# Optimization experiments

Hardware: AMD Instinct MI355X
Metric: run time of the kernel (lower is better)

## Reference

```python
import jax, jax.numpy as jnp
import numpy as np

N = 100000
E = 1600000
H = 2   # heads
C = 64  # per-head channels
NEG_SLOPE = 0.2


def setup_inputs() -> dict:
    key = jax.random.key(0)
    ks = jax.random.split(key, 12)
    s = 0.05
    return {
        "logits": jax.random.normal(ks[0], (N, 40), jnp.float32),
        "features": jax.random.normal(ks[1], (N, 256), jnp.float32),
        "edge_index": jax.random.randint(ks[2], (2, E), 0, N, jnp.int32),
        "W_feat": jax.random.normal(ks[3], (256, 128), jnp.float32) * s,
        "b_feat": jnp.zeros((128,), jnp.float32),
        "W0": jax.random.normal(ks[4], (168, 128), jnp.float32) * s,
        "att_src0": jax.random.normal(ks[5], (H, C), jnp.float32) * s,
        "att_dst0": jax.random.normal(ks[6], (H, C), jnp.float32) * s,
        "bias0": jnp.zeros((128,), jnp.float32),
        "W1": jax.random.normal(ks[7], (128, 128), jnp.float32) * s,
        "att_src1": jax.random.normal(ks[8], (H, C), jnp.float32) * s,
        "att_dst1": jax.random.normal(ks[9], (H, C), jnp.float32) * s,
        "bias1": jnp.zeros((128,), jnp.float32),
        "W_out": jax.random.normal(ks[10], (128, 40), jnp.float32) * s,
        "b_out": jnp.zeros((40,), jnp.float32),
    }


def gat_conv(x, src, dst, W, att_src, att_dst, bias):
    # x: [N, F_in] -> h: [N, H, C]
    h = (x @ W).reshape(N, H, C)
    a_src = (h * att_src).sum(-1)  # [N, H]
    a_dst = (h * att_dst).sum(-1)  # [N, H]
    # per-edge attention logits, leaky relu
    e = jax.nn.leaky_relu(a_src[src] + a_dst[dst], NEG_SLOPE)  # [E+N, H]
    # segment softmax over incoming edges of each dst node
    e_max = jax.ops.segment_max(e, dst, num_segments=N)
    e_exp = jnp.exp(e - e_max[dst])
    denom = jax.ops.segment_sum(e_exp, dst, num_segments=N)
    alpha = e_exp / (denom[dst] + 1e-16)  # [E+N, H]
    # weighted message aggregation (scatter-add)
    msg = h[src] * alpha[:, :, None]  # [E+N, H, C]
    out = jax.ops.segment_sum(msg, dst, num_segments=N)
    return out.reshape(N, H * C) + bias


def reference(logits, features, edge_index, W_feat, b_feat,
              W0, att_src0, att_dst0, bias0,
              W1, att_src1, att_dst1, bias1,
              W_out, b_out):
    # input assembly: [logits | proj(features)]
    x = jnp.concatenate([logits, features @ W_feat + b_feat], axis=-1)  # [N,168]
    # add self loops (PyG GATConv default add_self_loops=True)
    loops = jnp.arange(N, dtype=edge_index.dtype)
    src = jnp.concatenate([edge_index[0], loops])
    dst = jnp.concatenate([edge_index[1], loops])
    x = gat_conv(x, src, dst, W0, att_src0, att_dst0, bias0)
    x = jax.nn.relu(x)  # relu between conv layers (dropout=0 / eval)
    x = gat_conv(x, src, dst, W1, att_src1, att_dst1, bias1)
    return x @ W_out + b_out  # [N, 40]
```

## Files before the change

### kernel.cpp

```cpp
#include <hip/hip_runtime.h>

#define NN 100000
#define EE 1600000
#define NBUCK ((NN + 255) >> 8)
#define CHUNK 8192
#define NPBLK ((EE + CHUNK - 1) / CHUNK)

typedef __attribute__((ext_vector_type(8))) short short8_t;
typedef __attribute__((ext_vector_type(4))) float f32x4;

static __device__ inline unsigned short f2bf(float f) {
    unsigned int u = __float_as_uint(f);
    u += 0x7FFFu + ((u >> 16) & 1u);
    return (unsigned short)(u >> 16);
}
static __device__ inline float bf2f(unsigned short h) {
    return __uint_as_float(((unsigned int)h) << 16);
}

__global__ __launch_bounds__(256) void part_count(const int* __restrict__ ei,
                                                  int* __restrict__ cnt) {
    __shared__ int h[NBUCK];
    for (int i = threadIdx.x; i < NBUCK; i += 256) h[i] = 0;
    __syncthreads();
    int e0 = blockIdx.x * CHUNK;
    int e1 = e0 + CHUNK; if (e1 > EE) e1 = EE;
    for (int e = e0 + threadIdx.x; e < e1; e += 256)
        atomicAdd(&h[ei[EE + e] >> 8], 1);
    __syncthreads();
    for (int i = threadIdx.x; i < NBUCK; i += 256)
        cnt[blockIdx.x * NBUCK + i] = h[i];
}

__global__ void part_scan(const int* __restrict__ cnt, int* __restrict__ base,
                          int* __restrict__ bbase) {
    __shared__ int tot[512];
    int b = threadIdx.x;
    int t = 0;
    if (b < NBUCK)
        for (int k = 0; k < NPBLK; ++k) t += cnt[k * NBUCK + b];
    tot[b] = t;
    __syncthreads();
    for (int off = 1; off < 512; off <<= 1) {
        int u = (b >= off) ? tot[b - off] : 0;
        __syncthreads();
        tot[b] += u;
        __syncthreads();
    }
    int excl = tot[b] - t;
    if (b < NBUCK) {
        bbase[b] = excl;
        int run = excl;
        for (int k = 0; k < NPBLK; ++k) {
            base[k * NBUCK + b] = run;
            run += cnt[k * NBUCK + b];
        }
    }
    if (b == 0) bbase[NBUCK] = EE;
}

__global__ __launch_bounds__(256) void part_scatter(const int* __restrict__ ei,
                                                    const int* __restrict__ base,
                                                    unsigned int* __restrict__ bbuf) {
    __shared__ int lcur[NBUCK];
    for (int i = threadIdx.x; i < NBUCK; i += 256)
        lcur[i] = base[blockIdx.x * NBUCK + i];
    __syncthreads();
    int e0 = blockIdx.x * CHUNK;
    int e1 = e0 + CHUNK; if (e1 > EE) e1 = EE;
    for (int e = e0 + threadIdx.x; e < e1; e += 256) {
        int s = ei[e], d = ei[EE + e];
        int pos = atomicAdd(&lcur[d >> 8], 1);
        bbuf[pos] = (unsigned int)s | ((unsigned int)(d & 255) << 24);
    }
}

__global__ __launch_bounds__(256) void csr_build(const unsigned int* __restrict__ bbuf,
                                                 const int* __restrict__ bbase,
                                                 int* __restrict__ row_ptr,
                                                 int* __restrict__ col) {
    __shared__ int hist[256];
    __shared__ int sc[256];
    __shared__ int lcur[256];
    int b = blockIdx.x;
    int t = threadIdx.x;
    int n0 = b << 8;
    int nCnt = NN - n0; if (nCnt > 256) nCnt = 256;
    int es = bbase[b], ee2 = bbase[b + 1];
    hist[t] = 0;
    __syncthreads();
    for (int i = es + t; i < ee2; i += 256)
        atomicAdd(&hist[bbuf[i] >> 24], 1);
    __syncthreads();
    int v = hist[t];
    sc[t] = v;
    __syncthreads();
    for (int off = 1; off < 256; off <<= 1) {
        int u = (t >= off) ? sc[t - off] : 0;
        __syncthreads();
        sc[t] += u;
        __syncthreads();
    }
    int excl = sc[t] - v;
    if (t < nCnt) row_ptr[n0 + t] = es + excl;
    if (b == 0 && t == 0) row_ptr[NN] = EE;
    lcur[t] = excl;
    __syncthreads();
    for (int i = es + t; i < ee2; i += 256) {
        unsigned int pk = bbuf[i];
        int lpos = atomicAdd(&lcur[pk >> 24], 1);
        col[es + lpos] = (int)(pk & 0x00FFFFFFu);
    }
}

__global__ void bsplit_kernel(const float* __restrict__ W, int ldw, int K, int N,
                              unsigned short* __restrict__ BThi,
                              unsigned short* __restrict__ BTlo,
                              int stride, int koff, int KPseg) {
    int k = blockIdx.x * 256 + threadIdx.x;
    int col = blockIdx.y;
    if (k >= KPseg) return;
    float v = (k < K && col < N) ? W[(size_t)k * ldw + col] : 0.f;
    unsigned short hi = f2bf(v);
    unsigned short lo = f2bf(v - bf2f(hi));
    BThi[(size_t)col * stride + koff + k] = hi;
    BTlo[(size_t)col * stride + koff + k] = lo;
}

__global__ void cvec_kernel(const float* __restrict__ b_feat,
                            const float* __restrict__ W0, float* __restrict__ cvec) {
    int j = threadIdx.x;
    float s = 0.f;
    for (int k = 0; k < 128; ++k) s += b_feat[k] * W0[(40 + k) * 128 + j];
    cvec[j] = s;
}

#define AHI 0
#define ALO 2048
#define BHI 4096
#define BLO 8192
template <int OUTBF16, int ABF16>
__global__ __launch_bounds__(256) void mfma_gemm_kernel(
    const void* __restrict__ A1v, int lda1, int K1, int KP1,
    const float* __restrict__ A2, int lda2, int K2,
    int M,
    const unsigned short* __restrict__ BThi, const unsigned short* __restrict__ BTlo,
    int bstride, int KPtot,
    void* __restrict__ Cout, int ldc, int Nact, const float* __restrict__ bias)
{
    __shared__ __align__(16) unsigned short lds[12288];
    const int t = threadIdx.x;
    const int w = t >> 6, lane = t & 63;
    const int row0 = blockIdx.x * 64;
    const int rbase = (w & 1) * 32;
    const int cbase = (w >> 1) * 64;

    f32x4 acc[2][4];
#pragma unroll
    for (int i = 0; i < 2; ++i)
#pragma unroll
        for (int j = 0; j < 4; ++j) acc[i][j] = (f32x4){0.f, 0.f, 0.f, 0.f};

    const int arow = t >> 2;
    const int aslot = t & 3;
    const bool rowok = (row0 + arow) < M;
    const int aoff = arow * 32 + (((aslot ^ ((arow >> 1) & 3))) << 3);

    const int bc0 = t >> 2,        bs0 = t & 3;
    const int bc1 = (t + 256) >> 2, bs1 = (t + 256) & 3;
    const int bo0 = bc0 * 32 + ((bs0 ^ ((bc0 >> 1) & 3)) << 3);
    const int bo1 = bc1 * 32 + ((bs1 ^ ((bc1 >> 1) & 3)) << 3);

    float ra[8];
    short8_t rab;
    short8_t rbh0, rbl0, rbh1, rbl1;
    const short8_t zz = {0, 0, 0, 0, 0, 0, 0, 0};

#define LOADB(k0_) {                                                      \
        size_t g0_ = (size_t)bc0 * bstride + (k0_) + bs0 * 8;             \
        rbh0 = *(const short8_t*)&BThi[g0_];                              \
        rbl0 = *(const short8_t*)&BTlo[g0_];                              \
        size_t g1_ = (size_t)bc1 * bstride + (k0_) + bs1 * 8;             \
        rbh1 = *(const short8_t*)&BThi[g1_];                              \
        rbl1 = *(const short8_t*)&BTlo[g1_];                              \
    }

#define LOADA(k0_) {                                                      \
        if (ABF16) {                                                      \
            int gk = (k0_) + aslot * 8;                                   \
            if (rowok && gk + 8 <= K1) {                                  \
                const unsigned short* Ab =                                \
                    (const unsigned short*)A1v + (size_t)(row0 + arow) * lda1; \
                rab = *(const short8_t*)&Ab[gk];                          \
            } else rab = zz;                                              \
        } else {                                                          \
            const float* Asrc; int gk, Klim;                              \
            if ((k0_) < KP1) {                                            \
                Asrc = (const float*)A1v + (size_t)(row0 + arow) * lda1;  \
                gk = (k0_) + aslot * 8; Klim = K1;                        \
            } else {                                                      \
                Asrc = A2 + (size_t)(row0 + arow) * lda2;                 \
                gk = (k0_) - KP1 + aslot * 8; Klim = K2;                  \
            }                                                             \
            if (rowok && gk + 8 <= Klim) {                                \
                float4 v0 = *(const float4*)(Asrc + gk);                  \
                float4 v1 = *(const float4*)(Asrc + gk + 4);              \
                ra[0] = v0.x; ra[1] = v0.y; ra[2] = v0.z; ra[3] = v0.w;   \
                ra[4] = v1.x; ra[5] = v1.y; ra[6] = v1.z; ra[7] = v1.w;   \
            } else {                                                      \
                for (int j_ = 0; j_ < 8; ++j_) ra[j_] = 0.f;              \
            }                                                             \
        }                                                                 \
    }

    LOADA(0);
    LOADB(0);

    for (int k0 = 0; k0 < KPtot; k0 += 32) {
        if (ABF16) {
            *(short8_t*)&lds[AHI + aoff] = rab;
        } else {
            short8_t vh, vl;
#pragma unroll
            for (int j = 0; j < 8; ++j) {
                unsigned short hi = f2bf(ra[j]);
                vh[j] = (short)hi;
                vl[j] = (short)f2bf(ra[j] - bf2f(hi));
            }
            *(short8_t*)&lds[AHI + aoff] = vh;
            *(short8_t*)&lds[ALO + aoff] = vl;
        }
        *(short8_t*)&lds[BHI + bo0] = rbh0;
        *(short8_t*)&lds[BLO + bo0] = rbl0;
        *(short8_t*)&lds[BHI + bo1] = rbh1;
        *(short8_t*)&lds[BLO + bo1] = rbl1;
        __syncthreads();

        if (k0 + 32 < KPtot) {
            LOADA(k0 + 32);
            LOADB(k0 + 32);
        }

        short8_t Ah[2], Al[2], Bh[4], Bl[4];
        const int fslot = lane >> 4;
#pragma unroll
        for (int rt = 0; rt < 2; ++rt) {
            int r = rbase + rt * 16 + (lane & 15);
            int off = r * 32 + ((fslot ^ ((r >> 1) & 3)) << 3);
            Ah[rt] = *(const short8_t*)&lds[AHI + off];
            if (!ABF16) Al[rt] = *(const short8_t*)&lds[ALO + off];
        }
#pragma unroll
        for (int ct = 0; ct < 4; ++ct) {
            int c = cbase + ct * 16 + (lane & 15);
            int off = c * 32 + ((fslot ^ ((c >> 1) & 3)) << 3);
            Bh[ct] = *(const short8_t*)&lds[BHI + off];
            Bl[ct] = *(const short8_t*)&lds[BLO + off];
        }
#pragma unroll
        for (int rt = 0; rt < 2; ++rt)
#pragma unroll
            for (int ct = 0; ct < 4; ++ct) {
                acc[rt][ct] = __builtin_amdgcn_mfma_f32_16x16x32_bf16(Ah[rt], Bh[ct], acc[rt][ct], 0, 0, 0);
                acc[rt][ct] = __builtin_amdgcn_mfma_f32_16x16x32_bf16(Ah[rt], Bl[ct], acc[rt][ct], 0, 0, 0);
                if (!ABF16)
                    acc[rt][ct] = __builtin_amdgcn_mfma_f32_16x16x32_bf16(Al[rt], Bh[ct], acc[rt][ct], 0, 0, 0);
            }
        __syncthreads();
    }

#pragma unroll
    for (int rt = 0; rt < 2; ++rt) {
#pragma unroll
        for (int reg = 0; reg < 4; ++reg) {
            int r = row0 + rbase + rt * 16 + (lane >> 4) * 4 + reg;
            if (r >= M) continue;
#pragma unroll
            for (int ct = 0; ct < 4; ++ct) {
                int c = cbase + ct * 16 + (lane & 15);
                float v = acc[rt][ct][reg];
                if (bias) v += bias[c];
                if (OUTBF16) {
                    ((unsigned short*)Cout)[(size_t)r * 128 + c] = f2bf(v);
                } else {
                    if (c < Nact)
                        ((float*)Cout)[(size_t)r * ldc + c] = v;
                }
            }
        }
    }
#undef LOADA
#undef LOADB
}

__global__ void attn_coef_bf16(const unsigned short* __restrict__ hb,
                               const float* __restrict__ att_src,
                               const float* __restrict__ att_dst,
                               float* __restrict__ a_src, float* __restrict__ a_dst) {
    int n = (blockIdx.x * 256 + threadIdx.x) >> 6;
    if (n >= NN) return;
    int lane = threadIdx.x & 63;
    unsigned int hv = ((const unsigned int*)hb)[n * 64 + lane];
    float hx = __uint_as_float(hv << 16);
    float hy = __uint_as_float(hv & 0xFFFF0000u);
    int c0 = lane * 2;
    float vs = hx * att_src[c0] + hy * att_src[c0 + 1];
    float vd = hx * att_dst[c0] + hy * att_dst[c0 + 1];
#pragma unroll
    for (int off = 1; off <= 16; off <<= 1) {
        vs += __shfl_xor(vs, off);
        vd += __shfl_xor(vd, off);
    }
    if ((lane & 31) == 0) {
        int head = lane >> 5;
        a_src[n * 2 + head] = vs;
        a_dst[n * 2 + head] = vd;
    }
}

template <int RELU, int OUTBF16>
__global__ void gat_agg_fused(const int* __restrict__ row_ptr, const int* __restrict__ col,
                              const float* __restrict__ a_src, const float* __restrict__ a_dst,
                              const unsigned short* __restrict__ hb,
                              const float* __restrict__ bias, void* __restrict__ out) {
    int wid = (blockIdx.x * 256 + threadIdx.x) >> 6;
    if (wid >= NN) return;
    int lane = threadIdx.x & 63;
    int head = lane >> 5;
    const unsigned int* h2 = (const unsigned int*)hb;

    float2 ad = ((const float2*)a_dst)[wid];
    float2 asf = ((const float2*)a_src)[wid];
    float e0 = (head ? asf.y : asf.x) + (head ? ad.y : ad.x);
    e0 = e0 > 0.f ? e0 : 0.2f * e0;
    float w = __expf(e0);
    unsigned int hv = h2[wid * 64 + lane];
    float accx = w * __uint_as_float(hv << 16);
    float accy = w * __uint_as_float(hv & 0xFFFF0000u);
    float den = w;

    int rs = row_ptr[wid], re = row_ptr[wid + 1];
    for (int base = rs; base < re; base += 64) {
        int cnt = re - base;
        if (cnt > 64) cnt = 64;
        int sL = 0;
        float w0 = 0.f, w1 = 0.f;
        if (lane < cnt) {
            sL = col[base + lane];
            float2 as = ((const float2*)a_src)[sL];
            float t0 = as.x + ad.x;
            float t1 = as.y + ad.y;
            t0 = t0 > 0.f ? t0 : 0.2f * t0;
            t1 = t1 > 0.f ? t1 : 0.2f * t1;
            w0 = __expf(t0);
            w1 = __expf(t1);
        }
        int i = 0;
        for (; i + 8 <= cnt; i += 8) {
            int s[8];
            unsigned int g[8];
            float wa[8], wb[8];
#pragma unroll
            for (int j = 0; j < 8; ++j) s[j] = __shfl(sL, i + j);
#pragma unroll
            for (int j = 0; j < 8; ++j) g[j] = h2[s[j] * 64 + lane];
#pragma unroll
            for (int j = 0; j < 8; ++j) { wa[j] = __shfl(w0, i + j); wb[j] = __shfl(w1, i + j); }
#pragma unroll
            for (int j = 0; j < 8; ++j) {
                float ws = head ? wb[j] : wa[j];
                accx += ws * __uint_as_float(g[j] << 16);
                accy += ws * __uint_as_float(g[j] & 0xFFFF0000u);
                den += ws;
            }
        }
        for (; i + 4 <= cnt; i += 4) {
            int s[4];
            unsigned int g[4];
            float wa[4], wb[4];
#pragma unroll
            for (int j = 0; j < 4; ++j) s[j] = __shfl(sL, i + j);
#pragma unroll
            for (int j = 0; j < 4; ++j) g[j] = h2[s[j] * 64 + lane];
#pragma unroll
            for (int j = 0; j < 4; ++j) { wa[j] = __shfl(w0, i + j); wb[j] = __shfl(w1, i + j); }
#pragma unroll
            for (int j = 0; j < 4; ++j) {
                float ws = head ? wb[j] : wa[j];
                accx += ws * __uint_as_float(g[j] << 16);
                accy += ws * __uint_as_float(g[j] & 0xFFFF0000u);
                den += ws;
            }
        }
        for (; i < cnt; ++i) {
            int s = __shfl(sL, i);
            float wa = __shfl(w0, i);
            float wb = __shfl(w1, i);
            float ws = head ? wb : wa;
            unsigned int hs = h2[s * 64 + lane];
            accx += ws * __uint_as_float(hs << 16);
            accy += ws * __uint_as_float(hs & 0xFFFF0000u);
            den += ws;
        }
    }
    float inv = 1.f / (den + 1e-16f);
    float2 b2 = ((const float2*)bias)[lane];
    float ox = accx * inv + b2.x;
    float oy = accy * inv + b2.y;
    if (RELU) { ox = fmaxf(ox, 0.f); oy = fmaxf(oy, 0.f); }
    if (OUTBF16) {
        unsigned int pk = (unsigned int)f2bf(ox) | ((unsigned int)f2bf(oy) << 16);
        ((unsigned int*)out)[wid * 64 + lane] = pk;
    } else {
        ((float2*)out)[wid * 64 + lane] = make_float2(ox, oy);
    }
}

extern "C" void kernel_launch(void* const* d_in, const int* in_sizes, int n_in,
                              void* d_out, int out_size, void* d_ws, size_t ws_size,
                              hipStream_t stream) {
    const float* logits   = (const float*)d_in[0];
    const float* features = (const float*)d_in[1];
    const int*   ei       = (const int*)d_in[2];
    const float* W_feat   = (const float*)d_in[3];
    const float* b_feat   = (const float*)d_in[4];
    const float* W0       = (const float*)d_in[5];
    const float* att_src0 = (const float*)d_in[6];
    const float* att_dst0 = (const float*)d_in[7];
    const float* bias0    = (const float*)d_in[8];
    const float* W1       = (const float*)d_in[9];
    const float* att_src1 = (const float*)d_in[10];
    const float* att_dst1 = (const float*)d_in[11];
    const float* bias1    = (const float*)d_in[12];
    const float* W_out    = (const float*)d_in[13];
    const float* b_out    = (const float*)d_in[14];
    float* out = (float*)d_out;

    float* agg    = (float*)d_ws;
    float* a_srcb = agg + (size_t)NN * 128;
    float* a_dstb = a_srcb + (size_t)NN * 2;
    float* Wc     = a_dstb + (size_t)NN * 2;
    float* cvec   = Wc + 256 * 128;
    unsigned short* hbuf = (unsigned short*)(cvec + 128);
    unsigned short* BT0hi = hbuf + (size_t)NN * 128;
    unsigned short* BT0lo = BT0hi + 128 * 320;
    unsigned short* BTbhi = BT0lo + 128 * 320;
    unsigned short* BTblo = BTbhi + 128 * 128;
    unsigned short* BT1hi = BTblo + 128 * 128;
    unsigned short* BT1lo = BT1hi + 128 * 128;
    unsigned short* BTohi = BT1lo + 128 * 128;
    unsigned short* BTolo = BTohi + 128 * 128;
    int* row_ptr = (int*)(BTolo + 128 * 128);
    int* colbuf  = row_ptr + NN + 1;
    int* cnt     = colbuf + EE;
    int* pbase   = cnt + NPBLK * NBUCK;
    int* bbase   = pbase + NPBLK * NBUCK;
    unsigned int* bbuf = (unsigned int*)agg;
    unsigned short* aggb = (unsigned short*)agg;

    dim3 blk(256);
    const int gemmGrid = (NN + 63) / 64;
    const int nodeWaveGrid = (NN + 3) / 4;

    part_count<<<dim3(NPBLK), blk, 0, stream>>>(ei, cnt);
    part_scan<<<dim3(1), dim3(512), 0, stream>>>(cnt, pbase, bbase);
    part_scatter<<<dim3(NPBLK), blk, 0, stream>>>(ei, pbase, bbuf);
    csr_build<<<dim3(NBUCK), blk, 0, stream>>>(bbuf, bbase, row_ptr, colbuf);

    bsplit_kernel<<<dim3(1, 128), blk, 0, stream>>>(W0, 128, 40, 128, BT0hi, BT0lo, 320, 0, 64);
    bsplit_kernel<<<dim3(1, 128), blk, 0, stream>>>(W0 + 40 * 128, 128, 128, 128, BTbhi, BTblo, 128, 0, 128);
    mfma_gemm_kernel<0, 0><<<dim3(4), blk, 0, stream>>>(
        W_feat, 128, 128, 128, nullptr, 0, 0, 256,
        BTbhi, BTblo, 128, 128, Wc, 128, 128, nullptr);
    cvec_kernel<<<dim3(1), dim3(128), 0, stream>>>(b_feat, W0, cvec);
    bsplit_kernel<<<dim3(1, 128), blk, 0, stream>>>(Wc, 128, 256, 128, BT0hi, BT0lo, 320, 64, 256);
    bsplit_kernel<<<dim3(1, 128), blk, 0, stream>>>(W1, 128, 128, 128, BT1hi, BT1lo, 128, 0, 128);
    bsplit_kernel<<<dim3(1, 128), blk, 0, stream>>>(W_out, 40, 128, 40, BTohi, BTolo, 128, 0, 128);

    mfma_gemm_kernel<1, 0><<<dim3(gemmGrid), blk, 0, stream>>>(
        logits, 40, 40, 64, features, 256, 256, NN,
        BT0hi, BT0lo, 320, 320, hbuf, 128, 128, cvec);
    attn_coef_bf16<<<dim3(nodeWaveGrid), blk, 0, stream>>>(hbuf, att_src0, att_dst0, a_srcb, a_dstb);
    gat_agg_fused<1, 1><<<dim3(nodeWaveGrid), blk, 0, stream>>>(
        row_ptr, colbuf, a_srcb, a_dstb, hbuf, bias0, aggb);

    mfma_gemm_kernel<1, 1><<<dim3(gemmGrid), blk, 0, stream>>>(
        aggb, 128, 128, 128, nullptr, 0, 0, NN,
        BT1hi, BT1lo, 128, 128, hbuf, 128, 128, nullptr);
    attn_coef_bf16<<<dim3(nodeWaveGrid), blk, 0, stream>>>(hbuf, att_src1, att_dst1, a_srcb, a_dstb);
    gat_agg_fused<0, 0><<<dim3(nodeWaveGrid), blk, 0, stream>>>(
        row_ptr, colbuf, a_srcb, a_dstb, hbuf, bias1, agg);

    mfma_gemm_kernel<0, 0><<<dim3(gemmGrid), blk, 0, stream>>>(
        agg, 128, 128, 128, nullptr, 0, 0, NN,
        BTohi, BTolo, 128, 128, out, 40, 40, b_out);
}
```

Before: 332.5 us.

## Fuse attention coefficients into GEMM epilogue, double-buffer k-loop, trim output GEMM tiles

Attention-coefficient dot products are now computed in the MFMA GEMM epilogue from fp32 accumulators, which removes two separate kernels that re-read the bf16 h buffer. The GEMM k-loop is unrolled by two with two register prefetch buffers. The 40-column output GEMM uses a narrower column tile (NCT=2) so it skips unused B columns. The aggregation kernel now has each half-wave compute only its own head's edge weights over 32-edge chunks, which halves the exp work but doubles the number of chunk iterations. Attention coefficients now come from unrounded fp32 values instead of bf16 h, which slightly changes numerics, and the extra prefetch buffers raise register pressure.

```diff
diff --git a/kernel.cpp b/kernel.cpp
--- a/kernel.cpp
+++ b/kernel.cpp
@@ -139,60 +139,65 @@
 #define ALO 2048
 #define BHI 4096
 #define BLO 8192
-template <int OUTBF16, int ABF16>
+template <int OUTBF16, int ABF16, int ATTN, int NCT>
 __global__ __launch_bounds__(256) void mfma_gemm_kernel(
     const void* __restrict__ A1v, int lda1, int K1, int KP1,
     const float* __restrict__ A2, int lda2, int K2,
     int M,
     const unsigned short* __restrict__ BThi, const unsigned short* __restrict__ BTlo,
     int bstride, int KPtot,
-    void* __restrict__ Cout, int ldc, int Nact, const float* __restrict__ bias)
+    void* __restrict__ Cout, int ldc, int Nact, const float* __restrict__ bias,
+    const float* __restrict__ att_src, const float* __restrict__ att_dst,
+    float* __restrict__ a_srcO, float* __restrict__ a_dstO)
 {
     __shared__ __align__(16) unsigned short lds[12288];
     const int t = threadIdx.x;
     const int w = t >> 6, lane = t & 63;
     const int row0 = blockIdx.x * 64;
     const int rbase = (w & 1) * 32;
-    const int cbase = (w >> 1) * 64;
-
-    f32x4 acc[2][4];
+    const int cbase = (NCT == 4) ? (w >> 1) * 64 : (w >> 1) * 32;
+
+    f32x4 acc[2][NCT];
 #pragma unroll
     for (int i = 0; i < 2; ++i)
 #pragma unroll
-        for (int j = 0; j < 4; ++j) acc[i][j] = (f32x4){0.f, 0.f, 0.f, 0.f};
+        for (int j = 0; j < NCT; ++j) acc[i][j] = (f32x4){0.f, 0.f, 0.f, 0.f};
 
     const int arow = t >> 2;
     const int aslot = t & 3;
     const bool rowok = (row0 + arow) < M;
     const int aoff = arow * 32 + (((aslot ^ ((arow >> 1) & 3))) << 3);
 
-    const int bc0 = t >> 2,        bs0 = t & 3;
+    const int bc0 = t >> 2,         bs0 = t & 3;
     const int bc1 = (t + 256) >> 2, bs1 = (t + 256) & 3;
     const int bo0 = bc0 * 32 + ((bs0 ^ ((bc0 >> 1) & 3)) << 3);
     const int bo1 = bc1 * 32 + ((bs1 ^ ((bc1 >> 1) & 3)) << 3);
 
-    float ra[8];
-    short8_t rab;
-    short8_t rbh0, rbl0, rbh1, rbl1;
+    float ra0[8], ra1[8];
+    short8_t rab0, rab1;
+    short8_t bh0a, bl0a, bh1a, bl1a;
+    short8_t bh0b, bl0b, bh1b, bl1b;
     const short8_t zz = {0, 0, 0, 0, 0, 0, 0, 0};
 
-#define LOADB(k0_) {                                                      \
+#define LOADB_(k0_, H0, L0, H1, L1) {                                     \
         size_t g0_ = (size_t)bc0 * bstride + (k0_) + bs0 * 8;             \
-        rbh0 = *(const short8_t*)&BThi[g0_];                              \
-        rbl0 = *(const short8_t*)&BTlo[g0_];                              \
-        size_t g1_ = (size_t)bc1 * bstride + (k0_) + bs1 * 8;             \
-        rbh1 = *(const short8_t*)&BThi[g1_];                              \
-        rbl1 = *(const short8_t*)&BTlo[g1_];                              \
-    }
-
-#define LOADA(k0_) {                                                      \
+        H0 = *(const short8_t*)&BThi[g0_];                                \
+        L0 = *(const short8_t*)&BTlo[g0_];                                \
+        if (NCT == 4) {                                                   \
+            size_t g1_ = (size_t)bc1 * bstride + (k0_) + bs1 * 8;         \
+            H1 = *(const short8_t*)&BThi[g1_];                            \
+            L1 = *(const short8_t*)&BTlo[g1_];                            \
+        }                                                                 \
+    }
+
+#define LOADA_(k0_, RA, RAB) {                                            \
         if (ABF16) {                                                      \
             int gk = (k0_) + aslot * 8;                                   \
             if (rowok && gk + 8 <= K1) {                                  \
                 const unsigned short* Ab =                                \
                     (const unsigned short*)A1v + (size_t)(row0 + arow) * lda1; \
-                rab = *(const short8_t*)&Ab[gk];                          \
-            } else rab = zz;                                              \
+                RAB = *(const short8_t*)&Ab[gk];                          \
+            } else RAB = zz;                                              \
         } else {                                                          \
             const float* Asrc; int gk, Klim;                              \
             if ((k0_) < KP1) {                                            \
@@ -205,67 +210,81 @@
             if (rowok && gk + 8 <= Klim) {                                \
                 float4 v0 = *(const float4*)(Asrc + gk);                  \
                 float4 v1 = *(const float4*)(Asrc + gk + 4);              \
-                ra[0] = v0.x; ra[1] = v0.y; ra[2] = v0.z; ra[3] = v0.w;   \
-                ra[4] = v1.x; ra[5] = v1.y; ra[6] = v1.z; ra[7] = v1.w;   \
+                RA[0] = v0.x; RA[1] = v0.y; RA[2] = v0.z; RA[3] = v0.w;   \
+                RA[4] = v1.x; RA[5] = v1.y; RA[6] = v1.z; RA[7] = v1.w;   \
             } else {                                                      \
-                for (int j_ = 0; j_ < 8; ++j_) ra[j_] = 0.f;              \
+                for (int j_ = 0; j_ < 8; ++j_) RA[j_] = 0.f;              \
             }                                                             \
         }                                                                 \
     }
 
-    LOADA(0);
-    LOADB(0);
-
-    for (int k0 = 0; k0 < KPtot; k0 += 32) {
-        if (ABF16) {
-            *(short8_t*)&lds[AHI + aoff] = rab;
-        } else {
-            short8_t vh, vl;
-#pragma unroll
-            for (int j = 0; j < 8; ++j) {
-                unsigned short hi = f2bf(ra[j]);
-                vh[j] = (short)hi;
-                vl[j] = (short)f2bf(ra[j] - bf2f(hi));
-            }
-            *(short8_t*)&lds[AHI + aoff] = vh;
-            *(short8_t*)&lds[ALO + aoff] = vl;
-        }
-        *(short8_t*)&lds[BHI + bo0] = rbh0;
-        *(short8_t*)&lds[BLO + bo0] = rbl0;
-        *(short8_t*)&lds[BHI + bo1] = rbh1;
-        *(short8_t*)&lds[BLO + bo1] = rbl1;
-        __syncthreads();
-
-        if (k0 + 32 < KPtot) {
-            LOADA(k0 + 32);
-            LOADB(k0 + 32);
-        }
-
-        short8_t Ah[2], Al[2], Bh[4], Bl[4];
-        const int fslot = lane >> 4;
-#pragma unroll
-        for (int rt = 0; rt < 2; ++rt) {
-            int r = rbase + rt * 16 + (lane & 15);
-            int off = r * 32 + ((fslot ^ ((r >> 1) & 3)) << 3);
-            Ah[rt] = *(const short8_t*)&lds[AHI + off];
-            if (!ABF16) Al[rt] = *(const short8_t*)&lds[ALO + off];
-        }
-#pragma unroll
-        for (int ct = 0; ct < 4; ++ct) {
-            int c = cbase + ct * 16 + (lane & 15);
-            int off = c * 32 + ((fslot ^ ((c >> 1) & 3)) << 3);
-            Bh[ct] = *(const short8_t*)&lds[BHI + off];
-            Bl[ct] = *(const short8_t*)&lds[BLO + off];
-        }
-#pragma unroll
-        for (int rt = 0; rt < 2; ++rt)
-#pragma unroll
-            for (int ct = 0; ct < 4; ++ct) {
-                acc[rt][ct] = __builtin_amdgcn_mfma_f32_16x16x32_bf16(Ah[rt], Bh[ct], acc[rt][ct], 0, 0, 0);
-                acc[rt][ct] = __builtin_amdgcn_mfma_f32_16x16x32_bf16(Ah[rt], Bl[ct], acc[rt][ct], 0, 0, 0);
-                if (!ABF16)
-                    acc[rt][ct] = __builtin_amdgcn_mfma_f32_16x16x32_bf16(Al[rt], Bh[ct], acc[rt][ct], 0, 0, 0);
-            }
+#define STAGE_(RA, RAB, H0, L0, H1, L1) {                                 \
+        if (ABF16) {                                                      \
+            *(short8_t*)&lds[AHI + aoff] = RAB;                           \
+        } else {                                                          \
+            short8_t vh_, vl_;                                            \
+            for (int j_ = 0; j_ < 8; ++j_) {                              \
+                unsigned short hi_ = f2bf(RA[j_]);                        \
+                vh_[j_] = (short)hi_;                                     \
+                vl_[j_] = (short)f2bf(RA[j_] - bf2f(hi_));                \
+            }                                                             \
+            *(short8_t*)&lds[AHI + aoff] = vh_;                           \
+            *(short8_t*)&lds[ALO + aoff] = vl_;                           \
+        }                                                                 \
+        *(short8_t*)&lds[BHI + bo0] = H0;                                 \
+        *(short8_t*)&lds[BLO + bo0] = L0;                                 \
+        if (NCT == 4) {                                                   \
+            *(short8_t*)&lds[BHI + bo1] = H1;                             \
+            *(short8_t*)&lds[BLO + bo1] = L1;                             \
+        }                                                                 \
+    }
+
+#define COMPUTE_() {                                                      \
+        short8_t Ah[2], Al[2], Bh[NCT], Bl[NCT];                          \
+        const int fslot = lane >> 4;                                      \
+        for (int rt = 0; rt < 2; ++rt) {                                  \
+            int r = rbase + rt * 16 + (lane & 15);                        \
+            int off = r * 32 + ((fslot ^ ((r >> 1) & 3)) << 3);           \
+            Ah[rt] = *(const short8_t*)&lds[AHI + off];                   \
+            if (!ABF16) Al[rt] = *(const short8_t*)&lds[ALO + off];       \
+        }                                                                 \
+        for (int ct = 0; ct < NCT; ++ct) {                                \
+            int c = cbase + ct * 16 + (lane & 15);                        \
+            int off = c * 32 + ((fslot ^ ((c >> 1) & 3)) << 3);           \
+            Bh[ct] = *(const short8_t*)&lds[BHI + off];                   \
+            Bl[ct] = *(const short8_t*)&lds[BLO + off];                   \
+        }                                                                 \
+        for (int rt = 0; rt < 2; ++rt)                                    \
+            for (int ct = 0; ct < NCT; ++ct) {                            \
+                acc[rt][ct] = __builtin_amdgcn_mfma_f32_16x16x32_bf16(Ah[rt], Bh[ct], acc[rt][ct], 0, 0, 0); \
+                acc[rt][ct] = __builtin_amdgcn_mfma_f32_16x16x32_bf16(Ah[rt], Bl[ct], acc[rt][ct], 0, 0, 0); \
+                if (!ABF16)                                               \
+                    acc[rt][ct] = __builtin_amdgcn_mfma_f32_16x16x32_bf16(Al[rt], Bh[ct], acc[rt][ct], 0, 0, 0); \
+            }                                                             \
+    }
+
+    LOADA_(0, ra0, rab0);
+    LOADB_(0, bh0a, bl0a, bh1a, bl1a);
+    LOADA_(32, ra1, rab1);
+    LOADB_(32, bh0b, bl0b, bh1b, bl1b);
+
+    for (int k0 = 0; k0 < KPtot; k0 += 64) {
+        STAGE_(ra0, rab0, bh0a, bl0a, bh1a, bl1a);
+        __syncthreads();
+        if (k0 + 64 < KPtot) {
+            LOADA_(k0 + 64, ra0, rab0);
+            LOADB_(k0 + 64, bh0a, bl0a, bh1a, bl1a);
+        }
+        COMPUTE_();
+        __syncthreads();
+
+        STAGE_(ra1, rab1, bh0b, bl0b, bh1b, bl1b);
+        __syncthreads();
+        if (k0 + 96 < KPtot) {
+            LOADA_(k0 + 96, ra1, rab1);
+            LOADB_(k0 + 96, bh0b, bl0b, bh1b, bl1b);
+        }
+        COMPUTE_();
         __syncthreads();
     }
 
@@ -274,9 +293,28 @@
 #pragma unroll
         for (int reg = 0; reg < 4; ++reg) {
             int r = row0 + rbase + rt * 16 + (lane >> 4) * 4 + reg;
+            if (ATTN) {
+                float ps = 0.f, pd = 0.f;
+#pragma unroll
+                for (int ct = 0; ct < NCT; ++ct) {
+                    int c = cbase + ct * 16 + (lane & 15);
+                    ps += acc[rt][ct][reg] * att_src[c];
+                    pd += acc[rt][ct][reg] * att_dst[c];
+                }
+#pragma unroll
+                for (int off = 1; off < 16; off <<= 1) {
+                    ps += __shfl_xor(ps, off);
+                    pd += __shfl_xor(pd, off);
+                }
+                if (r < M && (lane & 15) == 0) {
+                    int head = w >> 1;
+                    a_srcO[r * 2 + head] = ps;
+                    a_dstO[r * 2 + head] = pd;
+                }
+            }
             if (r >= M) continue;
 #pragma unroll
-            for (int ct = 0; ct < 4; ++ct) {
+            for (int ct = 0; ct < NCT; ++ct) {
                 int c = cbase + ct * 16 + (lane & 15);
                 float v = acc[rt][ct][reg];
                 if (bias) v += bias[c];
@@ -289,33 +327,10 @@
             }
         }
     }
-#undef LOADA
-#undef LOADB
-}
-
-__global__ void attn_coef_bf16(const unsigned short* __restrict__ hb,
-                               const float* __restrict__ att_src,
-                               const float* __restrict__ att_dst,
-                               float* __restrict__ a_src, float* __restrict__ a_dst) {
-    int n = (blockIdx.x * 256 + threadIdx.x) >> 6;
-    if (n >= NN) return;
-    int lane = threadIdx.x & 63;
-    unsigned int hv = ((const unsigned int*)hb)[n * 64 + lane];
-    float hx = __uint_as_float(hv << 16);
-    float hy = __uint_as_float(hv & 0xFFFF0000u);
-    int c0 = lane * 2;
-    float vs = hx * att_src[c0] + hy * att_src[c0 + 1];
-    float vd = hx * att_dst[c0] + hy * att_dst[c0 + 1];
-#pragma unroll
-    for (int off = 1; off <= 16; off <<= 1) {
-        vs += __shfl_xor(vs, off);
-        vd += __shfl_xor(vd, off);
-    }
-    if ((lane & 31) == 0) {
-        int head = lane >> 5;
-        a_src[n * 2 + head] = vs;
-        a_dst[n * 2 + head] = vd;
-    }
+#undef LOADA_
+#undef LOADB_
+#undef STAGE_
+#undef COMPUTE_
 }
 
 template <int RELU, int OUTBF16>
@@ -326,77 +341,73 @@
     int wid = (blockIdx.x * 256 + threadIdx.x) >> 6;
     if (wid >= NN) return;
     int lane = threadIdx.x & 63;
-    int head = lane >> 5;
+    int hc = lane >> 5;
     const unsigned int* h2 = (const unsigned int*)hb;
 
     float2 ad = ((const float2*)a_dst)[wid];
     float2 asf = ((const float2*)a_src)[wid];
-    float e0 = (head ? asf.y : asf.x) + (head ? ad.y : ad.x);
+    float adh = hc ? ad.y : ad.x;
+    float e0 = (hc ? asf.y : asf.x) + adh;
     e0 = e0 > 0.f ? e0 : 0.2f * e0;
     float w = __expf(e0);
     unsigned int hv = h2[wid * 64 + lane];
     float accx = w * __uint_as_float(hv << 16);
     float accy = w * __uint_as_float(hv & 0xFFFF0000u);
     float den = w;
+    const int shbase = hc << 5;
 
     int rs = row_ptr[wid], re = row_ptr[wid + 1];
-    for (int base = rs; base < re; base += 64) {
+    for (int base = rs; base < re; base += 32) {
         int cnt = re - base;
-        if (cnt > 64) cnt = 64;
+        if (cnt > 32) cnt = 32;
+        int eidx = lane & 31;
         int sL = 0;
-        float w0 = 0.f, w1 = 0.f;
-        if (lane < cnt) {
-            sL = col[base + lane];
+        float wL = 0.f;
+        if (eidx < cnt) {
+            sL = col[base + eidx];
             float2 as = ((const float2*)a_src)[sL];
-            float t0 = as.x + ad.x;
-            float t1 = as.y + ad.y;
-            t0 = t0 > 0.f ? t0 : 0.2f * t0;
-            t1 = t1 > 0.f ? t1 : 0.2f * t1;
-            w0 = __expf(t0);
-            w1 = __expf(t1);
+            float tt = (hc ? as.y : as.x) + adh;
+            tt = tt > 0.f ? tt : 0.2f * tt;
+            wL = __expf(tt);
         }
         int i = 0;
         for (; i + 8 <= cnt; i += 8) {
             int s[8];
             unsigned int g[8];
-            float wa[8], wb[8];
-#pragma unroll
-            for (int j = 0; j < 8; ++j) s[j] = __shfl(sL, i + j);
+            float ws[8];
+#pragma unroll
+            for (int j = 0; j < 8; ++j) s[j] = __shfl(sL, shbase + i + j);
 #pragma unroll
             for (int j = 0; j < 8; ++j) g[j] = h2[s[j] * 64 + lane];
 #pragma unroll
-            for (int j = 0; j < 8; ++j) { wa[j] = __shfl(w0, i + j); wb[j] = __shfl(w1, i + j); }
+            for (int j = 0; j < 8; ++j) ws[j] = __shfl(wL, shbase + i + j);
 #pragma unroll
             for (int j = 0; j < 8; ++j) {
-                float ws = head ? wb[j] : wa[j];
-                accx += ws * __uint_as_float(g[j] << 16);
-                accy += ws * __uint_as_float(g[j] & 0xFFFF0000u);
-                den += ws;
+                accx += ws[j] * __uint_as_float(g[j] << 16);
+                accy += ws[j] * __uint_as_float(g[j] & 0xFFFF0000u);
+                den += ws[j];
             }
         }
         for (; i + 4 <= cnt; i += 4) {
             int s[4];
             unsigned int g[4];
-            float wa[4], wb[4];
-#pragma unroll
-            for (int j = 0; j < 4; ++j) s[j] = __shfl(sL, i + j);
+            float ws[4];
+#pragma unroll
+            for (int j = 0; j < 4; ++j) s[j] = __shfl(sL, shbase + i + j);
 #pragma unroll
             for (int j = 0; j < 4; ++j) g[j] = h2[s[j] * 64 + lane];
 #pragma unroll
-            for (int j = 0; j < 4; ++j) { wa[j] = __shfl(w0, i + j); wb[j] = __shfl(w1, i + j); }
+            for (int j = 0; j < 4; ++j) ws[j] = __shfl(wL, shbase + i + j);
 #pragma unroll
             for (int j = 0; j < 4; ++j) {
-                float ws = head ? wb[j] : wa[j];
-                accx += ws * __uint_as_float(g[j] << 16);
-                accy += ws * __uint_as_float(g[j] & 0xFFFF0000u);
-                den += ws;
+                accx += ws[j] * __uint_as_float(g[j] << 16);
+                accy += ws[j] * __uint_as_float(g[j] & 0xFFFF0000u);
+                den += ws[j];
             }
         }
         for (; i < cnt; ++i) {
-            int s = __shfl(sL, i);
-            float wa = __shfl(w0, i);
-            float wb = __shfl(w1, i);
-            float ws = head ? wb : wa;
+            int s = __shfl(sL, shbase + i);
+            float ws = __shfl(wL, shbase + i);
             unsigned int hs = h2[s * 64 + lane];
             accx += ws * __uint_as_float(hs << 16);
             accy += ws * __uint_as_float(hs & 0xFFFF0000u);
@@ -469,29 +480,31 @@
 
     bsplit_kernel<<<dim3(1, 128), blk, 0, stream>>>(W0, 128, 40, 128, BT0hi, BT0lo, 320, 0, 64);
     bsplit_kernel<<<dim3(1, 128), blk, 0, stream>>>(W0 + 40 * 128, 128, 128, 128, BTbhi, BTblo, 128, 0, 128);
-    mfma_gemm_kernel<0, 0><<<dim3(4), blk, 0, stream>>>(
+    mfma_gemm_kernel<0, 0, 0, 4><<<dim3(4), blk, 0, stream>>>(
         W_feat, 128, 128, 128, nullptr, 0, 0, 256,
-        BTbhi, BTblo, 128, 128, Wc, 128, 128, nullptr);
+        BTbhi, BTblo, 128, 128, Wc, 128, 128, nullptr,
+        nullptr, nullptr, nullptr, nullptr);
     cvec_kernel<<<dim3(1), dim3(128), 0, stream>>>(b_feat, W0, cvec);
     bsplit_kernel<<<dim3(1, 128), blk, 0, stream>>>(Wc, 128, 256, 128, BT0hi, BT0lo, 320, 64, 256);
     bsplit_kernel<<<dim3(1, 128), blk, 0, stream>>>(W1, 128, 128, 128, BT1hi, BT1lo, 128, 0, 128);
     bsplit_kernel<<<dim3(1, 128), blk, 0, stream>>>(W_out, 40, 128, 40, BTohi, BTolo, 128, 0, 128);
 
-    mfma_gemm_kernel<1, 0><<<dim3(gemmGrid), blk, 0, stream>>>(
+    mfma_gemm_kernel<1, 0, 1, 4><<<dim3(gemmGrid), blk, 0, stream>>>(
         logits, 40, 40, 64, features, 256, 256, NN,
-        BT0hi, BT0lo, 320, 320, hbuf, 128, 128, cvec);
-    attn_coef_bf16<<<dim3(nodeWaveGrid), blk, 0, stream>>>(hbuf, att_src0, att_dst0, a_srcb, a_dstb);
+        BT0hi, BT0lo, 320, 320, hbuf, 128, 128, cvec,
+        att_src0, att_dst0, a_srcb, a_dstb);
     gat_agg_fused<1, 1><<<dim3(nodeWaveGrid), blk, 0, stream>>>(
         row_ptr, colbuf, a_srcb, a_dstb, hbuf, bias0, aggb);
 
-    mfma_gemm_kernel<1, 1><<<dim3(gemmGrid), blk, 0, stream>>>(
+    mfma_gemm_kernel<1, 1, 1, 4><<<dim3(gemmGrid), blk, 0, stream>>>(
         aggb, 128, 128, 128, nullptr, 0, 0, NN,
-        BT1hi, BT1lo, 128, 128, hbuf, 128, 128, nullptr);
-    attn_coef_bf16<<<dim3(nodeWaveGrid), blk, 0, stream>>>(hbuf, att_src1, att_dst1, a_srcb, a_dstb);
+        BT1hi, BT1lo, 128, 128, hbuf, 128, 128, nullptr,
+        att_src1, att_dst1, a_srcb, a_dstb);
     gat_agg_fused<0, 0><<<dim3(nodeWaveGrid), blk, 0, stream>>>(
         row_ptr, colbuf, a_srcb, a_dstb, hbuf, bias1, agg);
 
-    mfma_gemm_kernel<0, 0><<<dim3(gemmGrid), blk, 0, stream>>>(
+    mfma_gemm_kernel<0, 0, 0, 2><<<dim3(gemmGrid), blk, 0, stream>>>(
         agg, 128, 128, 128, nullptr, 0, 0, NN,
-        BTohi, BTolo, 128, 128, out, 40, 40, b_out);
-}
+        BTohi, BTolo, 128, 128, out, 40, 40, b_out,
+        nullptr, nullptr, nullptr, nullptr);
+}
```

Result: faster. 316.2 us (-4.9%).
